# Kernel optimization log

Hardware: AMD Instinct MI355X
Metric: run time of the kernel (lower is better)

The kernel has to match this reference:

```python
import jax, jax.numpy as jnp
import numpy as np

N_NODES = 100000
N_EDGES = 1600000


def _graphconv(h, src, dst, norm_src, norm_dst, W, b, n_nodes):
    # DGL GraphConv, norm='both': D_dst^{-1/2} * A * (D_src^{-1/2} * h) @ W + b, then relu
    h = h * norm_src[:, None]
    agg = jax.ops.segment_sum(h[src], dst, num_segments=n_nodes)  # [N, d] SpMM
    rst = agg @ W  # in_feats <= out_feats path: aggregate first, then W
    rst = rst * norm_dst[:, None]
    rst = rst + b
    return jax.nn.relu(rst)


def setup_inputs() -> dict:
    key = jax.random.key(0)
    ks = jax.random.split(key, 12)
    H = 64
    features = jax.random.normal(ks[0], (N_NODES, H), dtype=jnp.float32)
    src = jax.random.randint(ks[1], (N_EDGES,), 0, N_NODES, dtype=jnp.int64 if jax.config.jax_enable_x64 else jnp.int32)
    dst = jax.random.randint(ks[2], (N_EDGES,), 0, N_NODES, dtype=jnp.int64 if jax.config.jax_enable_x64 else jnp.int32)
    sc = 1.0 / np.sqrt(H)
    W1 = jax.random.normal(ks[3], (H, H), dtype=jnp.float32) * sc
    b1 = jnp.zeros((H,), dtype=jnp.float32)
    W2 = jax.random.normal(ks[4], (H, H), dtype=jnp.float32) * sc
    b2 = jnp.zeros((H,), dtype=jnp.float32)
    W3 = jax.random.normal(ks[5], (H, H), dtype=jnp.float32) * sc
    b3 = jnp.zeros((H,), dtype=jnp.float32)
    Wc = jax.random.normal(ks[6], (H, 10), dtype=jnp.float32) * sc
    bc = jnp.zeros((10,), dtype=jnp.float32)
    return {"features": features, "src": src, "dst": dst,
            "W1": W1, "b1": b1, "W2": W2, "b2": b2, "W3": W3, "b3": b3,
            "Wc": Wc, "bc": bc}


def reference(features, src, dst, W1, b1, W2, b2, W3, b3, Wc, bc):
    n = features.shape[0]
    ones = jnp.ones_like(src, dtype=features.dtype)
    deg_out = jax.ops.segment_sum(ones, src, num_segments=n)
    deg_in = jax.ops.segment_sum(ones, dst, num_segments=n)
    norm_src = jnp.clip(deg_out, 1.0) ** -0.5  # allow_zero_in_degree: clamp(min=1)
    norm_dst = jnp.clip(deg_in, 1.0) ** -0.5
    h = features
    for W, b in ((W1, b1), (W2, b2), (W3, b3)):
        # dropout p=0.0 / eval mode -> identity
        h = _graphconv(h, src, dst, norm_src, norm_dst, W, b, n)
    hg = jnp.mean(h, axis=0, keepdims=True)  # AvgPooling over the single graph -> [1, H]
    logits = hg @ Wc + bc  # [1, n_classes]
    return (logits, hg)
```

## Files before the change

kernel.cpp:

```cpp
#include <hip/hip_runtime.h>
#include <hip/hip_fp8.h>


__global__ void build_kernel(const int* __restrict__ src, const int* __restrict__ dst,
                             int* __restrict__ deg_out, int* __restrict__ cursor,
                             int* __restrict__ csr_src, int E) {
  int i = blockIdx.x * blockDim.x + threadIdx.x;
  if (i < E) {
    int s = src[i];
    int d = dst[i];
    atomicAdd(&deg_out[s], 1);
    int p = atomicAdd(&cursor[d], 1);
    if (p < 64) csr_src[(size_t)d * 64 + p] = s;
  }
}

__global__ void pad_kernel(const int* __restrict__ cnt, int* __restrict__ csr_src, int N) {
  int i = blockIdx.x * blockDim.x + threadIdx.x;
  int n = i >> 6;
  int slot = i & 63;
  if (n < N) {
    int deg = min(cnt[n], 64);
    int pend = min((deg + 15) & ~15, 64);
    if (slot >= deg && slot < pend) csr_src[(size_t)n * 64 + slot] = N;
  }
}

__device__ __forceinline__ unsigned char f32_to_fp8(float f) {
  __hip_fp8_e4m3 q(f);
  return (unsigned char)q.__x;
}

__device__ __forceinline__ float fp8_to_f32(unsigned char v) {
  __hip_fp8_e4m3 q;
  q.__x = (__hip_fp8_storage_t)v;
  return (float)q;
}

__global__ __launch_bounds__(256) void gemm_scale_kernel(
    const float* __restrict__ h, const float* __restrict__ W,
    const int* __restrict__ deg_out, unsigned char* __restrict__ g, int N) {
  int lane = threadIdx.x & 63;
  int wave = (blockIdx.x << 2) + (threadIdx.x >> 6);
  int nwaves = gridDim.x << 2;
  float wcol[64];
#pragma unroll
  for (int k = 0; k < 64; k++) wcol[k] = W[k * 64 + lane];
  for (int n = wave; n < N; n += nwaves) {
    int nu = __builtin_amdgcn_readfirstlane(n);
    const float* __restrict__ hrow = h + (size_t)nu * 64;
    float acc = 0.f;
#pragma unroll
    for (int k = 0; k < 64; k++) acc = fmaf(hrow[k], wcol[k], acc);
    float val = acc * rsqrtf((float)max(deg_out[nu], 1));
    g[(size_t)nu * 64 + lane] = f32_to_fp8(val);
  }
}

#define GATHER16_FP8(base)                                                     \
  {                                                                            \
    int s0 = row[e + 0], s1 = row[e + 1], s2 = row[e + 2], s3 = row[e + 3];    \
    int s4 = row[e + 4], s5 = row[e + 5], s6 = row[e + 6], s7 = row[e + 7];    \
    int s8 = row[e + 8], s9 = row[e + 9], sa = row[e + 10], sb = row[e + 11];  \
    int sc = row[e + 12], sd = row[e + 13], se = row[e + 14], sf = row[e + 15];\
    unsigned char v0 = base[(size_t)s0 * 64 + lane];                           \
    unsigned char v1 = base[(size_t)s1 * 64 + lane];                           \
    unsigned char v2 = base[(size_t)s2 * 64 + lane];                           \
    unsigned char v3 = base[(size_t)s3 * 64 + lane];                           \
    unsigned char v4 = base[(size_t)s4 * 64 + lane];                           \
    unsigned char v5 = base[(size_t)s5 * 64 + lane];                           \
    unsigned char v6 = base[(size_t)s6 * 64 + lane];                           \
    unsigned char v7 = base[(size_t)s7 * 64 + lane];                           \
    unsigned char v8 = base[(size_t)s8 * 64 + lane];                           \
    unsigned char v9 = base[(size_t)s9 * 64 + lane];                           \
    unsigned char va = base[(size_t)sa * 64 + lane];                           \
    unsigned char vb = base[(size_t)sb * 64 + lane];                           \
    unsigned char vc = base[(size_t)sc * 64 + lane];                           \
    unsigned char vd = base[(size_t)sd * 64 + lane];                           \
    unsigned char ve = base[(size_t)se * 64 + lane];                           \
    unsigned char vf = base[(size_t)sf * 64 + lane];                           \
    acc += (((fp8_to_f32(v0) + fp8_to_f32(v1)) + (fp8_to_f32(v2) + fp8_to_f32(v3))) +   \
            ((fp8_to_f32(v4) + fp8_to_f32(v5)) + (fp8_to_f32(v6) + fp8_to_f32(v7)))) +  \
           (((fp8_to_f32(v8) + fp8_to_f32(v9)) + (fp8_to_f32(va) + fp8_to_f32(vb))) +   \
            ((fp8_to_f32(vc) + fp8_to_f32(vd)) + (fp8_to_f32(ve) + fp8_to_f32(vf))));   \
  }

__global__ __launch_bounds__(256) void spmm_kernel(
    const unsigned char* __restrict__ g, const int* __restrict__ cnt,
    const int* __restrict__ csr_src, const float* __restrict__ bias,
    float* __restrict__ h_out, int N) {
  int lane = threadIdx.x & 63;
  int wave = (blockIdx.x << 2) + (threadIdx.x >> 6);
  int nwaves = gridDim.x << 2;
  float b = bias[lane];
  for (int w1 = wave; w1 < N; w1 += nwaves) {
    int w = __builtin_amdgcn_readfirstlane(w1);
    int deg = min(cnt[w], 64);
    const int* __restrict__ row = csr_src + (size_t)w * 64;
    int end = min((deg + 15) & ~15, 64);
    float acc = 0.f;
    for (int e = 0; e < end; e += 16) GATHER16_FP8(g)
    float r = acc * rsqrtf((float)max(deg, 1)) + b;
    h_out[(size_t)w * 64 + lane] = fmaxf(r, 0.f);
  }
}

__global__ __launch_bounds__(256) void spmm_pool_kernel(
    const unsigned char* __restrict__ g, const int* __restrict__ cnt,
    const int* __restrict__ csr_src, const float* __restrict__ bias,
    float* __restrict__ pool, int N) {
  int lane = threadIdx.x & 63;
  int wid = threadIdx.x >> 6;
  int wave = (blockIdx.x << 2) + wid;
  int nwaves = gridDim.x << 2;
  float b = bias[lane];
  float psum = 0.f;
  for (int w1 = wave; w1 < N; w1 += nwaves) {
    int w = __builtin_amdgcn_readfirstlane(w1);
    int deg = min(cnt[w], 64);
    const int* __restrict__ row = csr_src + (size_t)w * 64;
    int end = min((deg + 15) & ~15, 64);
    float acc = 0.f;
    for (int e = 0; e < end; e += 16) GATHER16_FP8(g)
    psum += fmaxf(acc * rsqrtf((float)max(deg, 1)) + b, 0.f);
  }
  __shared__ float red[4][64];
  red[wid][lane] = psum;
  __syncthreads();
  if (wid == 0) {
    float v = red[0][lane] + red[1][lane] + red[2][lane] + red[3][lane];
    atomicAdd(&pool[lane], v);
  }
}

__global__ void final_kernel(const float* __restrict__ pool, const float* __restrict__ Wc,
                             const float* __restrict__ bc, float* __restrict__ out, float invN) {
  int t = threadIdx.x;
  __shared__ float hg[64];
  float m = pool[t] * invN;
  hg[t] = m;
  out[10 + t] = m;
  __syncthreads();
  if (t < 10) {
    float s = bc[t];
#pragma unroll
    for (int k = 0; k < 64; k++) s = fmaf(hg[k], Wc[k * 10 + t], s);
    out[t] = s;
  }
}

extern "C" void kernel_launch(void* const* d_in, const int* in_sizes, int n_in,
                              void* d_out, int out_size, void* d_ws, size_t ws_size,
                              hipStream_t stream) {
  const float* features = (const float*)d_in[0];
  const int* src = (const int*)d_in[1];
  const int* dst = (const int*)d_in[2];
  const float* W1 = (const float*)d_in[3];
  const float* b1 = (const float*)d_in[4];
  const float* W2 = (const float*)d_in[5];
  const float* b2 = (const float*)d_in[6];
  const float* W3 = (const float*)d_in[7];
  const float* b3 = (const float*)d_in[8];
  const float* Wc = (const float*)d_in[9];
  const float* bc = (const float*)d_in[10];
  float* out = (float*)d_out;

  const int N = in_sizes[0] / 64;
  const int E = in_sizes[1];

  char* ws = (char*)d_ws;
  size_t off = 0;
  auto alloc = [&](size_t bytes) {
    void* p = ws + off;
    off = (off + bytes + 255) & ~(size_t)255;
    return p;
  };
  int* deg_out = (int*)alloc((size_t)N * 4);
  int* cursor = (int*)alloc((size_t)N * 4);
  float* pool = (float*)alloc(64 * 4);
  size_t zero_bytes = off;
  int* csr_src = (int*)alloc((size_t)N * 64 * 4);
  unsigned char* bufG = (unsigned char*)alloc((size_t)(N + 1) * 64);
  float* bufH = (float*)alloc((size_t)N * 64 * 4);

  hipMemsetAsync(d_ws, 0, zero_bytes, stream);
  hipMemsetAsync(bufG + (size_t)N * 64, 0, 64, stream);

  int eb = (E + 255) / 256;
  build_kernel<<<eb, 256, 0, stream>>>(src, dst, deg_out, cursor, csr_src, E);
  pad_kernel<<<(N * 64 + 255) / 256, 256, 0, stream>>>(cursor, csr_src, N);

  gemm_scale_kernel<<<2048, 256, 0, stream>>>(features, W1, deg_out, bufG, N);
  spmm_kernel<<<2048, 256, 0, stream>>>(bufG, cursor, csr_src, b1, bufH, N);
  gemm_scale_kernel<<<2048, 256, 0, stream>>>(bufH, W2, deg_out, bufG, N);
  spmm_kernel<<<2048, 256, 0, stream>>>(bufG, cursor, csr_src, b2, bufH, N);
  gemm_scale_kernel<<<2048, 256, 0, stream>>>(bufH, W3, deg_out, bufG, N);
  spmm_pool_kernel<<<2048, 256, 0, stream>>>(bufG, cursor, csr_src, b3, pool, N);
  final_kernel<<<1, 64, 0, stream>>>(pool, Wc, bc, out, 1.0f / (float)N);
}
```

Before: 488.7 us.

## Load rows once per wave and broadcast via readlane; pad neighbor lists to 8

The GEMM now loads each h row with one coalesced vector load and broadcasts elements to all lanes with readlane, where before it issued 64 uniform scalar loads. The SpMM kernels likewise load the 64-entry neighbor index row into a VGPR and extract each index with readlane. Neighbor lists are now padded to multiples of 8 rather than 16, with an 8-wide tail gather, so fewer dummy gathers are issued for the average degree of about 16. The cost is many readlane instructions and some extra VALU/SALU serialization.

New measurement: 472.5 us. -3.3%, faster.

```diff
diff --git a/kernel.cpp b/kernel.cpp
--- a/kernel.cpp
+++ b/kernel.cpp
@@ -21,7 +21,7 @@
   int slot = i & 63;
   if (n < N) {
     int deg = min(cnt[n], 64);
-    int pend = min((deg + 15) & ~15, 64);
+    int pend = min((deg + 7) & ~7, 64);
     if (slot >= deg && slot < pend) csr_src[(size_t)n * 64 + slot] = N;
   }
 }
@@ -35,6 +35,10 @@
   __hip_fp8_e4m3 q;
   q.__x = (__hip_fp8_storage_t)v;
   return (float)q;
+}
+
+__device__ __forceinline__ float rl_f(float v, int srclane) {
+  return __uint_as_float(__builtin_amdgcn_readlane(__float_as_uint(v), srclane));
 }
 
 __global__ __launch_bounds__(256) void gemm_scale_kernel(
@@ -48,21 +52,33 @@
   for (int k = 0; k < 64; k++) wcol[k] = W[k * 64 + lane];
   for (int n = wave; n < N; n += nwaves) {
     int nu = __builtin_amdgcn_readfirstlane(n);
-    const float* __restrict__ hrow = h + (size_t)nu * 64;
+    float hval = h[(size_t)nu * 64 + lane];
     float acc = 0.f;
 #pragma unroll
-    for (int k = 0; k < 64; k++) acc = fmaf(hrow[k], wcol[k], acc);
+    for (int k = 0; k < 64; k++) acc = fmaf(rl_f(hval, k), wcol[k], acc);
     float val = acc * rsqrtf((float)max(deg_out[nu], 1));
     g[(size_t)nu * 64 + lane] = f32_to_fp8(val);
   }
 }
 
-#define GATHER16_FP8(base)                                                     \
+#define GATHER16_RL(base)                                                      \
   {                                                                            \
-    int s0 = row[e + 0], s1 = row[e + 1], s2 = row[e + 2], s3 = row[e + 3];    \
-    int s4 = row[e + 4], s5 = row[e + 5], s6 = row[e + 6], s7 = row[e + 7];    \
-    int s8 = row[e + 8], s9 = row[e + 9], sa = row[e + 10], sb = row[e + 11];  \
-    int sc = row[e + 12], sd = row[e + 13], se = row[e + 14], sf = row[e + 15];\
+    int s0 = __builtin_amdgcn_readlane(idxv, e + 0);                           \
+    int s1 = __builtin_amdgcn_readlane(idxv, e + 1);                           \
+    int s2 = __builtin_amdgcn_readlane(idxv, e + 2);                           \
+    int s3 = __builtin_amdgcn_readlane(idxv, e + 3);                           \
+    int s4 = __builtin_amdgcn_readlane(idxv, e + 4);                           \
+    int s5 = __builtin_amdgcn_readlane(idxv, e + 5);                           \
+    int s6 = __builtin_amdgcn_readlane(idxv, e + 6);                           \
+    int s7 = __builtin_amdgcn_readlane(idxv, e + 7);                           \
+    int s8 = __builtin_amdgcn_readlane(idxv, e + 8);                           \
+    int s9 = __builtin_amdgcn_readlane(idxv, e + 9);                           \
+    int sa = __builtin_amdgcn_readlane(idxv, e + 10);                          \
+    int sb = __builtin_amdgcn_readlane(idxv, e + 11);                          \
+    int sc = __builtin_amdgcn_readlane(idxv, e + 12);                          \
+    int sd = __builtin_amdgcn_readlane(idxv, e + 13);                          \
+    int se = __builtin_amdgcn_readlane(idxv, e + 14);                          \
+    int sf = __builtin_amdgcn_readlane(idxv, e + 15);                          \
     unsigned char v0 = base[(size_t)s0 * 64 + lane];                           \
     unsigned char v1 = base[(size_t)s1 * 64 + lane];                           \
     unsigned char v2 = base[(size_t)s2 * 64 + lane];                           \
@@ -85,6 +101,28 @@
             ((fp8_to_f32(vc) + fp8_to_f32(vd)) + (fp8_to_f32(ve) + fp8_to_f32(vf))));   \
   }
 
+#define GATHER8_RL(base)                                                       \
+  {                                                                            \
+    int s0 = __builtin_amdgcn_readlane(idxv, e + 0);                           \
+    int s1 = __builtin_amdgcn_readlane(idxv, e + 1);                           \
+    int s2 = __builtin_amdgcn_readlane(idxv, e + 2);                           \
+    int s3 = __builtin_amdgcn_readlane(idxv, e + 3);                           \
+    int s4 = __builtin_amdgcn_readlane(idxv, e + 4);                           \
+    int s5 = __builtin_amdgcn_readlane(idxv, e + 5);                           \
+    int s6 = __builtin_amdgcn_readlane(idxv, e + 6);                           \
+    int s7 = __builtin_amdgcn_readlane(idxv, e + 7);                           \
+    unsigned char v0 = base[(size_t)s0 * 64 + lane];                           \
+    unsigned char v1 = base[(size_t)s1 * 64 + lane];                           \
+    unsigned char v2 = base[(size_t)s2 * 64 + lane];                           \
+    unsigned char v3 = base[(size_t)s3 * 64 + lane];                           \
+    unsigned char v4 = base[(size_t)s4 * 64 + lane];                           \
+    unsigned char v5 = base[(size_t)s5 * 64 + lane];                           \
+    unsigned char v6 = base[(size_t)s6 * 64 + lane];                           \
+    unsigned char v7 = base[(size_t)s7 * 64 + lane];                           \
+    acc += ((fp8_to_f32(v0) + fp8_to_f32(v1)) + (fp8_to_f32(v2) + fp8_to_f32(v3))) +    \
+           ((fp8_to_f32(v4) + fp8_to_f32(v5)) + (fp8_to_f32(v6) + fp8_to_f32(v7)));     \
+  }
+
 __global__ __launch_bounds__(256) void spmm_kernel(
     const unsigned char* __restrict__ g, const int* __restrict__ cnt,
     const int* __restrict__ csr_src, const float* __restrict__ bias,
@@ -96,10 +134,12 @@
   for (int w1 = wave; w1 < N; w1 += nwaves) {
     int w = __builtin_amdgcn_readfirstlane(w1);
     int deg = min(cnt[w], 64);
-    const int* __restrict__ row = csr_src + (size_t)w * 64;
-    int end = min((deg + 15) & ~15, 64);
+    int idxv = csr_src[(size_t)w * 64 + lane];
+    int end = min((deg + 7) & ~7, 64);
     float acc = 0.f;
-    for (int e = 0; e < end; e += 16) GATHER16_FP8(g)
+    int e = 0;
+    for (; e + 16 <= end; e += 16) GATHER16_RL(g)
+    if (e < end) GATHER8_RL(g)
     float r = acc * rsqrtf((float)max(deg, 1)) + b;
     h_out[(size_t)w * 64 + lane] = fmaxf(r, 0.f);
   }
@@ -118,10 +158,12 @@
   for (int w1 = wave; w1 < N; w1 += nwaves) {
     int w = __builtin_amdgcn_readfirstlane(w1);
     int deg = min(cnt[w], 64);
-    const int* __restrict__ row = csr_src + (size_t)w * 64;
-    int end = min((deg + 15) & ~15, 64);
+    int idxv = csr_src[(size_t)w * 64 + lane];
+    int end = min((deg + 7) & ~7, 64);
     float acc = 0.f;
-    for (int e = 0; e < end; e += 16) GATHER16_FP8(g)
+    int e = 0;
+    for (; e + 16 <= end; e += 16) GATHER16_RL(g)
+    if (e < end) GATHER8_RL(g)
     psum += fmaxf(acc * rsqrtf((float)max(deg, 1)) + b, 0.f);
   }
   __shared__ float red[4][64];
```
